# Kernel tuning notes

Hardware: AMD Instinct MI355X
Metric: run time of the kernel (lower is better)

The kernel has to match this reference:

```python
import jax, jax.numpy as jnp
import numpy as np

C = 256   # descriptor_dim
H = 4     # num_heads
D = C // H  # head_dim = 64
B, N = 8, 2048


def _conv1x1(x, w, b):
    # 1x1 Conv1d == per-position linear over channels: x [B,C,N], w [O,C], b [O]
    return jnp.einsum('oc,bcn->bon', w, x) + b[None, :, None]


def setup_inputs() -> dict:
    key = jax.random.key(0)
    ks = jax.random.split(key, 11)
    s = 1.0 / np.sqrt(C)
    return {
        'query': jax.random.normal(ks[0], (B, C, N), dtype=jnp.float32),
        'key':   jax.random.normal(ks[1], (B, C, N), dtype=jnp.float32),
        'value': jax.random.normal(ks[2], (B, C, N), dtype=jnp.float32),
        'wq': jax.random.normal(ks[3], (C, C), dtype=jnp.float32) * s,
        'bq': jax.random.normal(ks[4], (C,), dtype=jnp.float32) * s,
        'wk': jax.random.normal(ks[5], (C, C), dtype=jnp.float32) * s,
        'bk': jax.random.normal(ks[6], (C,), dtype=jnp.float32) * s,
        'wv': jax.random.normal(ks[7], (C, C), dtype=jnp.float32) * s,
        'bv': jax.random.normal(ks[8], (C,), dtype=jnp.float32) * s,
        'wm': jax.random.normal(ks[9], (C, C), dtype=jnp.float32) * s,
        'bm': jax.random.normal(ks[10], (C,), dtype=jnp.float32) * s,
    }


def reference(query, key, value, wq, bq, wk, bk, wv, bv, wm, bm):
    b = query.shape[0]
    # project then view channels as (head_dim, num_heads) -- matches torch .view order
    q = _conv1x1(query, wq, bq).reshape(b, D, H, -1)   # [B,D,H,N]
    k = _conv1x1(key,   wk, bk).reshape(b, D, H, -1)   # [B,D,H,M]
    v = _conv1x1(value, wv, bv).reshape(b, D, H, -1)   # [B,D,H,M]
    scores = jnp.einsum('bdhn,bdhm->bhnm', q, k) / (D ** 0.5)
    probs = jax.nn.softmax(scores, axis=-1)            # [B,H,N,M]
    out = jnp.einsum('bhnm,bdhm->bdhn', probs, v)      # [B,D,H,N]
    out = out.reshape(b, D * H, -1)                    # [B,C,N]
    return _conv1x1(out, wm, bm)
```

## Files before the change

### kernel.cpp

```cpp
#include <hip/hip_runtime.h>
#include <hip/hip_bf16.h>

typedef float f32x4 __attribute__((ext_vector_type(4)));
typedef float f32x16 __attribute__((ext_vector_type(16)));
typedef __bf16 bf16x8 __attribute__((ext_vector_type(8)));
typedef __bf16 bf16x4 __attribute__((ext_vector_type(4)));
typedef unsigned int uint2v __attribute__((ext_vector_type(2)));

constexpr int B_ = 8, C_ = 256, N_ = 2048, H_ = 4, D_ = 64;
constexpr int BH_ = B_ * H_;
constexpr size_t PER_ = (size_t)BH_ * N_ * D_;
constexpr float LOG2E = 1.44269504088896340736f;

static __device__ __forceinline__ float fast_exp2(float x) {
#if __has_builtin(__builtin_amdgcn_exp2f)
  return __builtin_amdgcn_exp2f(x);
#else
  return exp2f(x);
#endif
}

static __device__ __forceinline__ void* swz(void* base, int row, int cb) {
  return (char*)base + row * 128 + (cb ^ ((row & 7) << 4));
}
static __device__ __forceinline__ const void* swz(const void* base, int row, int cb) {
  return (const char*)base + row * 128 + (cb ^ ((row & 7) << 4));
}

struct W4 {
  const float* s0; const float* s1; const float* s2; const float* s3;
  __bf16* d0; __bf16* d1; __bf16* d2; __bf16* d3;
};

__global__ __launch_bounds__(256) void wcvt_kernel(W4 p) {
  const int m = blockIdx.y;
  const float* src = m == 0 ? p.s0 : m == 1 ? p.s1 : m == 2 ? p.s2 : p.s3;
  __bf16* dst = m == 0 ? p.d0 : m == 1 ? p.d1 : m == 2 ? p.d2 : p.d3;
  const int f = blockIdx.x * 256 + threadIdx.x;
  const int o_blk = f >> 9;
  const int ks = (f >> 6) & 7;
  const int lane = f & 63;
  const int row = o_blk * 16 + (lane & 15);
  const int kbase = ks * 32 + (lane >> 4) * 8;
  bf16x8 v;
  if (m == 3) {
    for (int e = 0; e < 8; e++) {
      const int k = kbase + e;
      const int c = ((k & 63) << 2) | (k >> 6);
      v[e] = (__bf16)src[row * 256 + c];
    }
  } else {
    const int srow = ((row & 63) << 2) | (row >> 6);
    const float* s = src + srow * 256 + kbase;
    float4 a = *(const float4*)s;
    float4 b = *(const float4*)(s + 4);
    v[0] = (__bf16)a.x; v[1] = (__bf16)a.y; v[2] = (__bf16)a.z; v[3] = (__bf16)a.w;
    v[4] = (__bf16)b.x; v[5] = (__bf16)b.y; v[6] = (__bf16)b.z; v[7] = (__bf16)b.w;
  }
  *(bf16x8*)&dst[(size_t)f * 8] = v;
}

__global__ __launch_bounds__(256) void qkv_fused_kernel(
    const float* __restrict__ xq, const float* __restrict__ xk,
    const float* __restrict__ xv, const __bf16* __restrict__ wfq,
    const __bf16* __restrict__ wfk, const __bf16* __restrict__ wfv,
    const float* __restrict__ bq, const float* __restrict__ bk,
    const float* __restrict__ bv, __bf16* __restrict__ oq,
    __bf16* __restrict__ ok, __bf16* __restrict__ ov) {
  __shared__ __bf16 xlds[64][264];

  const int m = blockIdx.x >> 8;
  int inner = blockIdx.x & 255;
  inner = (inner & 7) * 32 + (inner >> 3);
  const int b = inner >> 5, nb = inner & 31;
  const int n0 = nb * 64;

  const float* xf = m == 0 ? xq : m == 1 ? xk : xv;
  const __bf16* wf = m == 0 ? wfq : m == 1 ? wfk : wfv;
  const float* bias = m == 0 ? bq : m == 1 ? bk : bv;
  __bf16* out = m == 0 ? oq : m == 1 ? ok : ov;
  const float scale = m == 0 ? 0.125f * LOG2E : 1.0f;

  const int t = threadIdx.x;
  {
    const int kl = t >> 4;
    const int nl = (t & 15) * 4;
    const float* src = xf + (size_t)b * C_ * N_ + n0 + nl;
    for (int it = 0; it < 16; it++) {
      const int k = it * 16 + kl;
      float4 f = *(const float4*)(src + (size_t)k * N_);
      xlds[nl + 0][k] = (__bf16)f.x;
      xlds[nl + 1][k] = (__bf16)f.y;
      xlds[nl + 2][k] = (__bf16)f.z;
      xlds[nl + 3][k] = (__bf16)f.w;
    }
  }
  __syncthreads();

  const int lane = t & 63, wvv = t >> 6;
  const int wm = wvv >> 1, wn = wvv & 1;
  const int l15 = lane & 15, lg = lane >> 4;

  f32x4 acc[8][2] = {};

  for (int ks = 0; ks < 8; ks++) {
    bf16x8 bfr[2];
    for (int ni = 0; ni < 2; ni++)
      bfr[ni] = *(const bf16x8*)&xlds[wn * 32 + ni * 16 + l15][ks * 32 + lg * 8];
    for (int mi = 0; mi < 8; mi++) {
      bf16x8 af = *(const bf16x8*)&wf[(((size_t)(wm * 8 + mi) * 8 + ks) * 64 + lane) * 8];
      acc[mi][0] = __builtin_amdgcn_mfma_f32_16x16x32_bf16(af, bfr[0], acc[mi][0], 0, 0, 0);
      acc[mi][1] = __builtin_amdgcn_mfma_f32_16x16x32_bf16(af, bfr[1], acc[mi][1], 0, 0, 0);
    }
  }

  for (int mi = 0; mi < 8; mi++) {
    const int h = wm * 2 + (mi >> 2);
    const int d0 = (mi & 3) * 16 + 4 * lg;
    for (int ni = 0; ni < 2; ni++) {
      const int n = n0 + wn * 32 + ni * 16 + l15;
      if (m != 2) {
        bf16x4 o4;
        for (int r = 0; r < 4; r++)
          o4[r] = (__bf16)((acc[mi][ni][r] + bias[((d0 + r) << 2) | h]) * scale);
        *(bf16x4*)&out[((size_t)(b * H_ + h) * N_ + n) * D_ + d0] = o4;
      } else {
        for (int r = 0; r < 4; r++)
          out[((size_t)(b * H_ + h) * D_ + d0 + r) * N_ + n] =
              (__bf16)(acc[mi][ni][r] + bias[((d0 + r) << 2) | h]);
      }
    }
  }
}

__global__ __launch_bounds__(256) void final_proj_kernel(
    const __bf16* __restrict__ xb, const __bf16* __restrict__ wf,
    const float* __restrict__ bias, float* __restrict__ out) {
  const int bid = blockIdx.x;
  const int wid = (bid & 7) * 128 + (bid >> 3);
  const int o_t = wid & 3;
  const int nb = (wid >> 2) & 31;
  const int b = wid >> 7;
  const int o0 = o_t * 64, n0 = nb * 64;
  const int t = threadIdx.x, lane = t & 63;
  const int wvv = t >> 6, wm = wvv >> 1, wn = wvv & 1;
  const int l15 = lane & 15, lg = lane >> 4;
  const int nbase = n0 + wn * 32 + l15;

  f32x4 acc[2][2] = {};

  for (int ks = 0; ks < 8; ks++) {
    bf16x8 af[2];
    for (int mi = 0; mi < 2; mi++)
      af[mi] = *(const bf16x8*)&wf[(((size_t)(o_t * 4 + wm * 2 + mi) * 8 + ks) * 64 + lane) * 8];
    bf16x8 bfr[2];
    const size_t bh = (size_t)(b * H_ + (ks >> 1));
    const int d0 = (ks & 1) * 32 + lg * 8;
    for (int ni = 0; ni < 2; ni++)
      bfr[ni] = *(const bf16x8*)&xb[(bh * N_ + nbase + ni * 16) * D_ + d0];
    for (int mi = 0; mi < 2; mi++)
      for (int ni = 0; ni < 2; ni++)
        acc[mi][ni] = __builtin_amdgcn_mfma_f32_16x16x32_bf16(
            af[mi], bfr[ni], acc[mi][ni], 0, 0, 0);
  }

  for (int mi = 0; mi < 2; mi++) {
    for (int r = 0; r < 4; r++) {
      const int och = o0 + wm * 32 + mi * 16 + 4 * lg + r;
      const float bv_ = bias[och];
      for (int ni = 0; ni < 2; ni++) {
        const int n = n0 + wn * 32 + ni * 16 + l15;
        out[((size_t)b * C_ + och) * N_ + n] = acc[mi][ni][r] + bv_;
      }
    }
  }
}

template <int SPLIT>
__global__ __launch_bounds__(256) void attn_kernel(
    const __bf16* __restrict__ qb, const __bf16* __restrict__ kb,
    const __bf16* __restrict__ vtb, __bf16* __restrict__ pO,
    float* __restrict__ lbuf) {
  __shared__ __bf16 kbuf[2][64][64];
  __shared__ __bf16 vtbuf[2][64][64];

  const int t = threadIdx.x, lane = t & 63, wv = t >> 6;
  const int l31 = lane & 31, hi = lane >> 5;

  const int bid = blockIdx.x;
  const int s = (SPLIT > 1) ? (bid >> 9) : 0;
  const int inner = bid & 511;
  const int wid = (inner & 7) * 64 + (inner >> 3);
  const int bh = wid >> 4;
  const int qn = (wid & 15) * 128 + wv * 32;
  const int jbase = s * (N_ / SPLIT);
  constexpr int NT = N_ / SPLIT / 64;

  const __bf16* k_bh = kb + (size_t)bh * N_ * D_;
  const __bf16* vt_bh = vtb + (size_t)bh * D_ * N_;

  const __bf16* qrow = qb + ((size_t)bh * N_ + qn + l31) * D_;
  bf16x8 qf[4];
#pragma unroll
  for (int i = 0; i < 4; i++) qf[i] = *(const bf16x8*)(qrow + i * 16 + hi * 8);

  const int srow = t >> 2, sce = (t & 3) * 16;

  {
    uint4 ka = *(const uint4*)(k_bh + (size_t)(jbase + srow) * D_ + sce);
    uint4 kc = *(const uint4*)(k_bh + (size_t)(jbase + srow) * D_ + sce + 8);
    uint4 va = *(const uint4*)(vt_bh + (size_t)srow * N_ + jbase + sce);
    uint4 vc = *(const uint4*)(vt_bh + (size_t)srow * N_ + jbase + sce + 8);
    *(uint4*)swz(&kbuf[0][0][0], srow, sce * 2) = ka;
    *(uint4*)swz(&kbuf[0][0][0], srow, sce * 2 + 16) = kc;
    *(uint4*)swz(&vtbuf[0][0][0], srow, sce * 2) = va;
    *(uint4*)swz(&vtbuf[0][0][0], srow, sce * 2 + 16) = vc;
  }
  __syncthreads();

  f32x16 o0 = {}, o1 = {};
  float la0 = 0.f, la1 = 0.f, la2 = 0.f, la3 = 0.f;
  int cur = 0;

  for (int jt = 0; jt < NT; jt++) {
    const int j0 = jbase + jt * 64;
    const bool have = (jt + 1) < NT;
    uint4 pka, pkc, pva, pvc;
    if (have) {
      const int jn = j0 + 64;
      pka = *(const uint4*)(k_bh + (size_t)(jn + srow) * D_ + sce);
      pkc = *(const uint4*)(k_bh + (size_t)(jn + srow) * D_ + sce + 8);
      pva = *(const uint4*)(vt_bh + (size_t)srow * N_ + jn + sce);
      pvc = *(const uint4*)(vt_bh + (size_t)srow * N_ + jn + sce + 8);
    }

    f32x16 s0 = {}, s1 = {};
    __builtin_amdgcn_s_setprio(1);
#pragma unroll
    for (int i = 0; i < 4; i++) {
      bf16x8 kf = *(const bf16x8*)swz(&kbuf[cur][0][0], l31, i * 32 + hi * 16);
      s0 = __builtin_amdgcn_mfma_f32_32x32x16_bf16(kf, qf[i], s0, 0, 0, 0);
    }
#pragma unroll
    for (int i = 0; i < 4; i++) {
      bf16x8 kf = *(const bf16x8*)swz(&kbuf[cur][0][0], 32 + l31, i * 32 + hi * 16);
      s1 = __builtin_amdgcn_mfma_f32_32x32x16_bf16(kf, qf[i], s1, 0, 0, 0);
    }
    __builtin_amdgcn_s_setprio(0);

#pragma unroll
    for (int sub = 0; sub < 2; sub++) {
      const f32x16 sv = sub ? s1 : s0;
      float pr[16];
#pragma unroll
      for (int r = 0; r < 16; r++) pr[r] = fast_exp2(sv[r]);
      la0 += pr[0] + pr[4] + pr[8] + pr[12];
      la1 += pr[1] + pr[5] + pr[9] + pr[13];
      la2 += pr[2] + pr[6] + pr[10] + pr[14];
      la3 += pr[3] + pr[7] + pr[11] + pr[15];
      unsigned w[8];
#pragma unroll
      for (int g = 0; g < 8; g++) {
        union { __bf16 h[2]; unsigned u; } cv;
        cv.h[0] = (__bf16)pr[2 * g];
        cv.h[1] = (__bf16)pr[2 * g + 1];
        w[g] = cv.u;
      }
      uint2v r0 = __builtin_amdgcn_permlane32_swap(w[0], w[2], false, false);
      uint2v r1 = __builtin_amdgcn_permlane32_swap(w[1], w[3], false, false);
      uint2v r2 = __builtin_amdgcn_permlane32_swap(w[4], w[6], false, false);
      uint2v r3 = __builtin_amdgcn_permlane32_swap(w[5], w[7], false, false);
      union { unsigned u[4]; bf16x8 v; } f0 = {{r0.x, r1.x, r0.y, r1.y}};
      union { unsigned u[4]; bf16x8 v; } f1 = {{r2.x, r3.x, r2.y, r3.y}};
      const int scb = sub * 64;
      __builtin_amdgcn_s_setprio(1);
      {
        bf16x8 vf = *(const bf16x8*)swz(&vtbuf[cur][0][0], l31, scb + hi * 16);
        o0 = __builtin_amdgcn_mfma_f32_32x32x16_bf16(vf, f0.v, o0, 0, 0, 0);
        vf = *(const bf16x8*)swz(&vtbuf[cur][0][0], l31, scb + 32 + hi * 16);
        o0 = __builtin_amdgcn_mfma_f32_32x32x16_bf16(vf, f1.v, o0, 0, 0, 0);
        vf = *(const bf16x8*)swz(&vtbuf[cur][0][0], 32 + l31, scb + hi * 16);
        o1 = __builtin_amdgcn_mfma_f32_32x32x16_bf16(vf, f0.v, o1, 0, 0, 0);
        vf = *(const bf16x8*)swz(&vtbuf[cur][0][0], 32 + l31, scb + 32 + hi * 16);
        o1 = __builtin_amdgcn_mfma_f32_32x32x16_bf16(vf, f1.v, o1, 0, 0, 0);
      }
      __builtin_amdgcn_s_setprio(0);
    }

    if (have) {
      const int nxt = cur ^ 1;
      *(uint4*)swz(&kbuf[nxt][0][0], srow, sce * 2) = pka;
      *(uint4*)swz(&kbuf[nxt][0][0], srow, sce * 2 + 16) = pkc;
      *(uint4*)swz(&vtbuf[nxt][0][0], srow, sce * 2) = pva;
      *(uint4*)swz(&vtbuf[nxt][0][0], srow, sce * 2 + 16) = pvc;
      __syncthreads();
    }
    cur ^= 1;
  }

  float la = la0 + la1 + la2 + la3;
  la += __shfl_xor(la, 32);
  const float scl = (SPLIT == 1) ? 1.f / la : 1.f;

  if constexpr (SPLIT > 1) {
    if (hi == 0)
      lbuf[(size_t)s * BH_ * N_ + (size_t)bh * N_ + qn + l31] = la;
  }

  __syncthreads();
  char* ep = (char*)&vtbuf[0][0][0] + wv * 4096;
#pragma unroll
  for (int dt = 0; dt < 2; dt++) {
    const f32x16 o = dt ? o1 : o0;
#pragma unroll
    for (int g = 0; g < 4; g++) {
      bf16x4 o4;
#pragma unroll
      for (int j = 0; j < 4; j++) o4[j] = (__bf16)(o[4 * g + j] * scl);
      *(bf16x4*)swz(ep, l31, dt * 64 + 16 * g + 8 * hi) = o4;
    }
  }
  asm volatile("" ::: "memory");
  {
    __bf16* dst = pO + (size_t)s * PER_ + ((size_t)bh * N_ + qn) * D_;
#pragma unroll
    for (int i = 0; i < 4; i++) {
      const int row = i * 8 + (lane >> 3);
      uint4 v = *(const uint4*)swz(ep, row, (lane & 7) * 16);
      *(uint4*)((char*)dst + i * 1024 + lane * 16) = v;
    }
  }
}

__global__ __launch_bounds__(256) void combine_kernel(
    const __bf16* __restrict__ p0, const __bf16* __restrict__ p1,
    const float* __restrict__ l0, const float* __restrict__ l1,
    __bf16* __restrict__ outp) {
  const size_t idx8 = (size_t)blockIdx.x * 256 + threadIdx.x;
  const size_t nidx = idx8 >> 3;
  bf16x8 a = *(const bf16x8*)&p0[idx8 * 8];
  bf16x8 b = *(const bf16x8*)&p1[idx8 * 8];
  const float inv = 1.f / (l0[nidx] + l1[nidx]);
  bf16x8 r;
#pragma unroll
  for (int e = 0; e < 8; e++) r[e] = (__bf16)(((float)a[e] + (float)b[e]) * inv);
  *(bf16x8*)&outp[idx8 * 8] = r;
}

extern "C" void kernel_launch(void* const* d_in, const int* in_sizes, int n_in,
                              void* d_out, int out_size, void* d_ws,
                              size_t ws_size, hipStream_t stream) {
  const float* query = (const float*)d_in[0];
  const float* key_ = (const float*)d_in[1];
  const float* value = (const float*)d_in[2];
  const float* wq = (const float*)d_in[3];
  const float* bq = (const float*)d_in[4];
  const float* wk = (const float*)d_in[5];
  const float* bk = (const float*)d_in[6];
  const float* wv = (const float*)d_in[7];
  const float* bv = (const float*)d_in[8];
  const float* wm = (const float*)d_in[9];
  const float* bm = (const float*)d_in[10];

  __bf16* qb = (__bf16*)d_ws;
  __bf16* kb = qb + PER_;
  __bf16* vtb = kb + PER_;
  __bf16* p0 = vtb + PER_;
  __bf16* p1 = p0 + PER_;
  float* lbuf = (float*)(p1 + PER_);
  __bf16* wfq = (__bf16*)(lbuf + 2 * BH_ * N_);
  __bf16* wfk = wfq + 65536;
  __bf16* wfv = wfk + 65536;
  __bf16* wfm = wfv + 65536;

  const size_t need_split = (size_t)((char*)(wfm + 65536) - (char*)d_ws);
  const bool use_split = ws_size >= need_split;

  dim3 blk(256);
  W4 wp{wq, wk, wv, wm, wfq, wfk, wfv, wfm};
  if (!use_split) {
    wfq = p1; wfk = wfq + 65536; wfv = wfk + 65536; wfm = wfv + 65536;
    wp = W4{wq, wk, wv, wm, wfq, wfk, wfv, wfm};
  }
  wcvt_kernel<<<dim3(32, 4), blk, 0, stream>>>(wp);

  qkv_fused_kernel<<<768, blk, 0, stream>>>(query, key_, value, wfq, wfk, wfv,
                                            bq, bk, bv, qb, kb, vtb);
  if (use_split) {
    attn_kernel<2><<<1024, blk, 0, stream>>>(qb, kb, vtb, p0, lbuf);
    combine_kernel<<<2048, blk, 0, stream>>>(p0, p1, lbuf, lbuf + BH_ * N_, p0);
  } else {
    attn_kernel<1><<<512, blk, 0, stream>>>(qb, kb, vtb, p0, nullptr);
  }
  final_proj_kernel<<<1024, blk, 0, stream>>>(p0, wfm, bm, (float*)d_out);
}
```

Before: 107.5 us.

## Pre-swizzle K/V tiles in projection and stream them via global_load_lds

Measured after the change: 98.42 us. 1.09x faster.

```diff
diff --git a/kernel.cpp b/kernel.cpp
--- a/kernel.cpp
+++ b/kernel.cpp
@@ -6,6 +6,7 @@
 typedef __bf16 bf16x8 __attribute__((ext_vector_type(8)));
 typedef __bf16 bf16x4 __attribute__((ext_vector_type(4)));
 typedef unsigned int uint2v __attribute__((ext_vector_type(2)));
+typedef unsigned int u32;
 
 constexpr int B_ = 8, C_ = 256, N_ = 2048, H_ = 4, D_ = 64;
 constexpr int BH_ = B_ * H_;
@@ -25,6 +26,12 @@
 }
 static __device__ __forceinline__ const void* swz(const void* base, int row, int cb) {
   return (const char*)base + row * 128 + (cb ^ ((row & 7) << 4));
+}
+
+static __device__ __forceinline__ void gload16(void* lds, const void* g) {
+  __builtin_amdgcn_global_load_lds(
+      (const __attribute__((address_space(1))) u32*)g,
+      (__attribute__((address_space(3))) u32*)lds, 16, 0, 0);
 }
 
 struct W4 {
@@ -66,7 +73,7 @@
     const __bf16* __restrict__ wfk, const __bf16* __restrict__ wfv,
     const float* __restrict__ bq, const float* __restrict__ bk,
     const float* __restrict__ bv, __bf16* __restrict__ oq,
-    __bf16* __restrict__ ok, __bf16* __restrict__ ov) {
+    char* __restrict__ oksw, char* __restrict__ ovsw) {
   __shared__ __bf16 xlds[64][264];
 
   const int m = blockIdx.x >> 8;
@@ -78,7 +85,6 @@
   const float* xf = m == 0 ? xq : m == 1 ? xk : xv;
   const __bf16* wf = m == 0 ? wfq : m == 1 ? wfk : wfv;
   const float* bias = m == 0 ? bq : m == 1 ? bk : bv;
-  __bf16* out = m == 0 ? oq : m == 1 ? ok : ov;
   const float scale = m == 0 ? 0.125f * LOG2E : 1.0f;
 
   const int t = threadIdx.x;
@@ -119,14 +125,20 @@
     const int d0 = (mi & 3) * 16 + 4 * lg;
     for (int ni = 0; ni < 2; ni++) {
       const int n = n0 + wn * 32 + ni * 16 + l15;
-      if (m != 2) {
+      const size_t tbase = ((size_t)(b * H_ + h) * (N_ / 64) + (n >> 6)) * 8192;
+      if (m == 0) {
         bf16x4 o4;
         for (int r = 0; r < 4; r++)
           o4[r] = (__bf16)((acc[mi][ni][r] + bias[((d0 + r) << 2) | h]) * scale);
-        *(bf16x4*)&out[((size_t)(b * H_ + h) * N_ + n) * D_ + d0] = o4;
+        *(bf16x4*)&oq[((size_t)(b * H_ + h) * N_ + n) * D_ + d0] = o4;
+      } else if (m == 1) {
+        bf16x4 o4;
+        for (int r = 0; r < 4; r++)
+          o4[r] = (__bf16)(acc[mi][ni][r] + bias[((d0 + r) << 2) | h]);
+        *(bf16x4*)swz(oksw + tbase, n & 63, 2 * d0) = o4;
       } else {
         for (int r = 0; r < 4; r++)
-          out[((size_t)(b * H_ + h) * D_ + d0 + r) * N_ + n] =
+          *(__bf16*)swz(ovsw + tbase, d0 + r, 2 * (n & 63)) =
               (__bf16)(acc[mi][ni][r] + bias[((d0 + r) << 2) | h]);
       }
     }
@@ -177,45 +189,41 @@
 }
 
 template <int SPLIT>
-__global__ __launch_bounds__(256) void attn_kernel(
-    const __bf16* __restrict__ qb, const __bf16* __restrict__ kb,
-    const __bf16* __restrict__ vtb, __bf16* __restrict__ pO,
+__global__ __launch_bounds__(512) void attn_kernel(
+    const __bf16* __restrict__ qb, const char* __restrict__ kbsw,
+    const char* __restrict__ vtsw, __bf16* __restrict__ pO,
     float* __restrict__ lbuf) {
-  __shared__ __bf16 kbuf[2][64][64];
-  __shared__ __bf16 vtbuf[2][64][64];
+  __shared__ char smem[32768];
 
   const int t = threadIdx.x, lane = t & 63, wv = t >> 6;
   const int l31 = lane & 31, hi = lane >> 5;
 
   const int bid = blockIdx.x;
-  const int s = (SPLIT > 1) ? (bid >> 9) : 0;
-  const int inner = bid & 511;
-  const int wid = (inner & 7) * 64 + (inner >> 3);
-  const int bh = wid >> 4;
-  const int qn = (wid & 15) * 128 + wv * 32;
-  const int jbase = s * (N_ / SPLIT);
+  const int per_xcd = (256 * SPLIT) / 8;
+  const int wid = (bid & 7) * per_xcd + (bid >> 3);
+  const int bh = wid / (8 * SPLIT);
+  const int rem = wid % (8 * SPLIT);
+  const int qt = rem & 7;
+  const int s = rem >> 3;
+  const int qn = qt * 256 + wv * 32;
   constexpr int NT = N_ / SPLIT / 64;
-
-  const __bf16* k_bh = kb + (size_t)bh * N_ * D_;
-  const __bf16* vt_bh = vtb + (size_t)bh * D_ * N_;
+  const int jt0 = s * NT;
+
+  const char* ktiles = kbsw + (size_t)bh * (N_ / 64) * 8192;
+  const char* vtiles = vtsw + (size_t)bh * (N_ / 64) * 8192;
 
   const __bf16* qrow = qb + ((size_t)bh * N_ + qn + l31) * D_;
   bf16x8 qf[4];
 #pragma unroll
   for (int i = 0; i < 4; i++) qf[i] = *(const bf16x8*)(qrow + i * 16 + hi * 8);
 
-  const int srow = t >> 2, sce = (t & 3) * 16;
-
-  {
-    uint4 ka = *(const uint4*)(k_bh + (size_t)(jbase + srow) * D_ + sce);
-    uint4 kc = *(const uint4*)(k_bh + (size_t)(jbase + srow) * D_ + sce + 8);
-    uint4 va = *(const uint4*)(vt_bh + (size_t)srow * N_ + jbase + sce);
-    uint4 vc = *(const uint4*)(vt_bh + (size_t)srow * N_ + jbase + sce + 8);
-    *(uint4*)swz(&kbuf[0][0][0], srow, sce * 2) = ka;
-    *(uint4*)swz(&kbuf[0][0][0], srow, sce * 2 + 16) = kc;
-    *(uint4*)swz(&vtbuf[0][0][0], srow, sce * 2) = va;
-    *(uint4*)swz(&vtbuf[0][0][0], srow, sce * 2 + 16) = vc;
-  }
+  auto stage = [&](int jt_g, int bb) {
+    gload16(smem + bb * 8192 + t * 16, ktiles + (size_t)jt_g * 8192 + t * 16);
+    gload16(smem + 16384 + bb * 8192 + t * 16,
+            vtiles + (size_t)jt_g * 8192 + t * 16);
+  };
+
+  stage(jt0, 0);
   __syncthreads();
 
   f32x16 o0 = {}, o1 = {};
@@ -223,27 +231,20 @@
   int cur = 0;
 
   for (int jt = 0; jt < NT; jt++) {
-    const int j0 = jbase + jt * 64;
-    const bool have = (jt + 1) < NT;
-    uint4 pka, pkc, pva, pvc;
-    if (have) {
-      const int jn = j0 + 64;
-      pka = *(const uint4*)(k_bh + (size_t)(jn + srow) * D_ + sce);
-      pkc = *(const uint4*)(k_bh + (size_t)(jn + srow) * D_ + sce + 8);
-      pva = *(const uint4*)(vt_bh + (size_t)srow * N_ + jn + sce);
-      pvc = *(const uint4*)(vt_bh + (size_t)srow * N_ + jn + sce + 8);
-    }
+    if (jt + 1 < NT) stage(jt0 + jt + 1, cur ^ 1);
+    const char* kc = smem + cur * 8192;
+    const char* vc = smem + 16384 + cur * 8192;
 
     f32x16 s0 = {}, s1 = {};
     __builtin_amdgcn_s_setprio(1);
 #pragma unroll
     for (int i = 0; i < 4; i++) {
-      bf16x8 kf = *(const bf16x8*)swz(&kbuf[cur][0][0], l31, i * 32 + hi * 16);
+      bf16x8 kf = *(const bf16x8*)swz(kc, l31, i * 32 + hi * 16);
       s0 = __builtin_amdgcn_mfma_f32_32x32x16_bf16(kf, qf[i], s0, 0, 0, 0);
     }
 #pragma unroll
     for (int i = 0; i < 4; i++) {
-      bf16x8 kf = *(const bf16x8*)swz(&kbuf[cur][0][0], 32 + l31, i * 32 + hi * 16);
+      bf16x8 kf = *(const bf16x8*)swz(kc, 32 + l31, i * 32 + hi * 16);
       s1 = __builtin_amdgcn_mfma_f32_32x32x16_bf16(kf, qf[i], s1, 0, 0, 0);
     }
     __builtin_amdgcn_s_setprio(0);
@@ -275,26 +276,19 @@
       const int scb = sub * 64;
       __builtin_amdgcn_s_setprio(1);
       {
-        bf16x8 vf = *(const bf16x8*)swz(&vtbuf[cur][0][0], l31, scb + hi * 16);
+        bf16x8 vf = *(const bf16x8*)swz(vc, l31, scb + hi * 16);
         o0 = __builtin_amdgcn_mfma_f32_32x32x16_bf16(vf, f0.v, o0, 0, 0, 0);
-        vf = *(const bf16x8*)swz(&vtbuf[cur][0][0], l31, scb + 32 + hi * 16);
+        vf = *(const bf16x8*)swz(vc, l31, scb + 32 + hi * 16);
         o0 = __builtin_amdgcn_mfma_f32_32x32x16_bf16(vf, f1.v, o0, 0, 0, 0);
-        vf = *(const bf16x8*)swz(&vtbuf[cur][0][0], 32 + l31, scb + hi * 16);
+        vf = *(const bf16x8*)swz(vc, 32 + l31, scb + hi * 16);
         o1 = __builtin_amdgcn_mfma_f32_32x32x16_bf16(vf, f0.v, o1, 0, 0, 0);
-        vf = *(const bf16x8*)swz(&vtbuf[cur][0][0], 32 + l31, scb + 32 + hi * 16);
+        vf = *(const bf16x8*)swz(vc, 32 + l31, scb + 32 + hi * 16);
         o1 = __builtin_amdgcn_mfma_f32_32x32x16_bf16(vf, f1.v, o1, 0, 0, 0);
       }
       __builtin_amdgcn_s_setprio(0);
     }
 
-    if (have) {
-      const int nxt = cur ^ 1;
-      *(uint4*)swz(&kbuf[nxt][0][0], srow, sce * 2) = pka;
-      *(uint4*)swz(&kbuf[nxt][0][0], srow, sce * 2 + 16) = pkc;
-      *(uint4*)swz(&vtbuf[nxt][0][0], srow, sce * 2) = pva;
-      *(uint4*)swz(&vtbuf[nxt][0][0], srow, sce * 2 + 16) = pvc;
-      __syncthreads();
-    }
+    __syncthreads();
     cur ^= 1;
   }
 
@@ -307,8 +301,7 @@
       lbuf[(size_t)s * BH_ * N_ + (size_t)bh * N_ + qn + l31] = la;
   }
 
-  __syncthreads();
-  char* ep = (char*)&vtbuf[0][0][0] + wv * 4096;
+  char* ep = smem + wv * 4096;
 #pragma unroll
   for (int dt = 0; dt < 2; dt++) {
     const f32x16 o = dt ? o1 : o0;
@@ -363,9 +356,9 @@
   const float* bm = (const float*)d_in[10];
 
   __bf16* qb = (__bf16*)d_ws;
-  __bf16* kb = qb + PER_;
-  __bf16* vtb = kb + PER_;
-  __bf16* p0 = vtb + PER_;
+  char* kbsw = (char*)(qb + PER_);
+  char* vtsw = kbsw + PER_ * 2;
+  __bf16* p0 = (__bf16*)(vtsw + PER_ * 2);
   __bf16* p1 = p0 + PER_;
   float* lbuf = (float*)(p1 + PER_);
   __bf16* wfq = (__bf16*)(lbuf + 2 * BH_ * N_);
@@ -385,12 +378,12 @@
   wcvt_kernel<<<dim3(32, 4), blk, 0, stream>>>(wp);
 
   qkv_fused_kernel<<<768, blk, 0, stream>>>(query, key_, value, wfq, wfk, wfv,
-                                            bq, bk, bv, qb, kb, vtb);
+                                            bq, bk, bv, qb, kbsw, vtsw);
   if (use_split) {
-    attn_kernel<2><<<1024, blk, 0, stream>>>(qb, kb, vtb, p0, lbuf);
+    attn_kernel<2><<<512, dim3(512), 0, stream>>>(qb, kbsw, vtsw, p0, lbuf);
     combine_kernel<<<2048, blk, 0, stream>>>(p0, p1, lbuf, lbuf + BH_ * N_, p0);
   } else {
-    attn_kernel<1><<<512, blk, 0, stream>>>(qb, kb, vtb, p0, nullptr);
+    attn_kernel<1><<<256, dim3(512), 0, stream>>>(qb, kbsw, vtsw, p0, nullptr);
   }
   final_proj_kernel<<<1024, blk, 0, stream>>>(p0, wfm, bm, (float*)d_out);
 }
```
